# Kernel tuning notes

Measured on AMD Instinct MI355X. Metric: run time of the kernel, lower is better.

The kernel has to match this reference:

```python
import jax, jax.numpy as jnp
import numpy as np

GROUP_DIMS = (128, 64, 128, 64)  # per-group feature widths, sum = 384
ATTN_OUT = 64                    # per-group attention output width
B, W = 65536, 3                  # batch, words (4 groups * 3 words * 64 = 768 = linear_inner in-features)


def setup_inputs() -> dict:
    key = jax.random.key(0)
    keys = iter(jax.random.split(key, 64))
    s = 0.02
    inp = {"words": jax.random.normal(next(keys), (B, W, sum(GROUP_DIMS)), jnp.float32)}
    for g, d in enumerate(GROUP_DIMS):
        inp[f"wqkv{g}"] = jax.random.normal(next(keys), (d, 3 * d), jnp.float32) * s
        inp[f"bqkv{g}"] = jnp.zeros((3 * d,), jnp.float32)
        inp[f"wo{g}"] = jax.random.normal(next(keys), (d, ATTN_OUT), jnp.float32) * s
        inp[f"bo{g}"] = jnp.zeros((ATTN_OUT,), jnp.float32)
    inp["wi"] = jax.random.normal(next(keys), (ATTN_OUT * 12, 256), jnp.float32) * s
    inp["bi"] = jnp.zeros((256,), jnp.float32)
    inp["wout"] = jax.random.normal(next(keys), (256, 1), jnp.float32) * s
    inp["bout"] = jnp.zeros((1,), jnp.float32)
    return inp


def _group_attn(x, wqkv, bqkv, wo, bo, d):
    # x: [B, W, d] -> self-attention over W words within this feature group
    qkv = x @ wqkv + bqkv                      # [B, W, 3d]
    q, k, v = jnp.split(qkv, 3, axis=-1)       # each [B, W, d]
    scores = jnp.einsum('bqd,bkd->bqk', q, k) / jnp.sqrt(jnp.float32(d))
    attn = jax.nn.softmax(scores, axis=-1)     # [B, W, W]
    out = jnp.einsum('bqk,bkd->bqd', attn, v)  # [B, W, d]
    return out @ wo + bo                       # [B, W, ATTN_OUT]


def reference(words, wqkv0, bqkv0, wo0, bo0, wqkv1, bqkv1, wo1, bo1,
              wqkv2, bqkv2, wo2, bo2, wqkv3, bqkv3, wo3, bo3,
              wi, bi, wout, bout):
    gp = [(wqkv0, bqkv0, wo0, bo0), (wqkv1, bqkv1, wo1, bo1),
          (wqkv2, bqkv2, wo2, bo2), (wqkv3, bqkv3, wo3, bo3)]
    outs, start = [], 0
    for (wqkv, bqkv, wo, bo), d in zip(gp, GROUP_DIMS):
        outs.append(_group_attn(words[..., start:start + d], wqkv, bqkv, wo, bo, d))
        start += d
    cat = jnp.concatenate(outs, axis=-2)                 # [B, 12, 64]
    flat = jax.nn.relu(cat.reshape(cat.shape[0], -1))    # [B, 768]
    inner = jax.nn.relu(flat @ wi + bi)                  # [B, 256]
    return inner @ wout + bout                           # [B, 1]
```

## Files before the change

### kernel.cpp

```cpp
#include <hip/hip_runtime.h>

typedef _Float16 f16;
typedef _Float16 half8 __attribute__((ext_vector_type(8)));
typedef _Float16 half4 __attribute__((ext_vector_type(4)));
typedef __fp16 fp16x2 __attribute__((ext_vector_type(2)));
typedef float f32x4 __attribute__((ext_vector_type(4)));

#define BTOT 65536

static const size_t OFF_FLAT = 0;
static const size_t SZ_FLAT  = (size_t)BTOT * 768 * 2;
static const size_t OFF_WIT  = OFF_FLAT + SZ_FLAT;
static const size_t SZ_WIT   = (size_t)256 * 768 * 2;
static const size_t SZ_WT128 = (size_t)208 * 128 * 2;
static const size_t SZ_WT64  = (size_t)144 * 64 * 2;
static const size_t OFF_WT0  = OFF_WIT + SZ_WIT;
static const size_t OFF_WT1  = OFF_WT0 + SZ_WT128;
static const size_t OFF_WT2  = OFF_WT1 + SZ_WT64;
static const size_t OFF_WT3  = OFF_WT2 + SZ_WT128;
static const size_t OFF_CO   = OFF_WT3 + SZ_WT64;
static const size_t OFF_C    = OFF_CO + 256 * 4;

__device__ __forceinline__ half4 cvt4(float4 v) {
    fp16x2 lo = __builtin_amdgcn_cvt_pkrtz(v.x, v.y);
    fp16x2 hi = __builtin_amdgcn_cvt_pkrtz(v.z, v.w);
    half4 h;
    h[0] = (_Float16)lo[0]; h[1] = (_Float16)lo[1];
    h[2] = (_Float16)hi[0]; h[3] = (_Float16)hi[1];
    return h;
}

__device__ __forceinline__ void ldsbar() {
    asm volatile("s_waitcnt lgkmcnt(0)" ::: "memory");
    __builtin_amdgcn_s_barrier();
    __builtin_amdgcn_sched_barrier(0);
}

__global__ __launch_bounds__(256) void pk_fuse(
    const float* __restrict__ wq0, const float* __restrict__ bq0, const float* __restrict__ wo0, const float* __restrict__ bo0,
    const float* __restrict__ wq1, const float* __restrict__ bq1, const float* __restrict__ wo1, const float* __restrict__ bo1,
    const float* __restrict__ wq2, const float* __restrict__ bq2, const float* __restrict__ wo2, const float* __restrict__ bo2,
    const float* __restrict__ wq3, const float* __restrict__ bq3, const float* __restrict__ wo3, const float* __restrict__ bo3,
    f16* __restrict__ wT0, f16* __restrict__ wT1, f16* __restrict__ wT2, f16* __restrict__ wT3,
    float* __restrict__ coAll, float* __restrict__ cAll)
{
    const int g = blockIdx.y;
    const float* wqkv; const float* bqkv; const float* wo; const float* bo; f16* wT; int D;
    switch (g) {
        case 0:  wqkv = wq0; bqkv = bq0; wo = wo0; bo = bo0; wT = wT0; D = 128; break;
        case 1:  wqkv = wq1; bqkv = bq1; wo = wo1; bo = bo1; wT = wT1; D = 64;  break;
        case 2:  wqkv = wq2; bqkv = bq2; wo = wo2; bo = bo2; wT = wT2; D = 128; break;
        default: wqkv = wq3; bqkv = bq3; wo = wo3; bo = bo3; wT = wT3; D = 64;  break;
    }
    const int sh = (D == 128) ? 7 : 6;
    const int NT = (D + 81) / 16;
    const int NTD = (NT * 16) << sh;
    const int total = NTD + 65;
    const int o = blockIdx.x * 256 + threadIdx.x;
    if (o >= total) return;
    const int s3 = 3 * D;
    const float sc = rsqrtf((float)D);
    if (o < NTD) {
        const int n = o >> sh, k = o & (D - 1);
        float val = 0.f;
        if (n < D) {
            const float* a = wqkv + (size_t)k * s3;
            const float* b = wqkv + (size_t)n * s3 + D;
            float s = 0.f;
            for (int m = 0; m < D; ++m) s += a[m] * b[m];
            val = s * sc;
        } else if (n < D + 64) {
            const int j = n - D;
            const float* a = wqkv + (size_t)k * s3 + 2 * D;
            float s = 0.f;
            for (int m = 0; m < D; ++m) s += a[m] * wo[m * 64 + j];
            val = s;
        } else if (n == D + 64) {
            const float* a = wqkv + (size_t)k * s3;
            float s = 0.f;
            for (int m = 0; m < D; ++m) s += a[m] * bqkv[D + m];
            val = s * sc;
        } else if (n == D + 65) {
            const float* a = wqkv + (size_t)k * s3 + D;
            float s = 0.f;
            for (int m = 0; m < D; ++m) s += a[m] * bqkv[m];
            val = s * sc;
        }
        wT[o] = (f16)val;
    } else if (o < NTD + 64) {
        const int j = o - NTD;
        float s = 0.f;
        for (int m = 0; m < D; ++m) s += bqkv[2 * D + m] * wo[m * 64 + j];
        coAll[g * 64 + j] = s + bo[j];
    } else {
        float s = 0.f;
        for (int m = 0; m < D; ++m) s += bqkv[m] * bqkv[D + m];
        cAll[g] = s * sc;
    }
}

__global__ __launch_bounds__(256) void pk_wit(const float* __restrict__ wi, f16* __restrict__ wiT)
{
    int o = blockIdx.x * 256 + threadIdx.x;
    int n = o / 768, k = o - n * 768;
    wiT[o] = (f16)wi[k * 256 + n];
}

template<int D>
__device__ __forceinline__ void run_group(
    const float* __restrict__ words, const f16* __restrict__ wT,
    const float* __restrict__ coAll, const float* __restrict__ cAll, int gidx,
    f16* __restrict__ flat, int tile, int start, int gbase, int t, char* smem)
{
    constexpr int KST = D / 32;
    constexpr int NT  = (D + 81) / 16;
    constexpr int XP  = D + 8;
    constexpr int F4  = D / 4;
    constexpr int NLD = 48 * F4 / 256;

    f16 (*Xs)[XP]  = (f16(*)[XP])(smem);
    f16 (*Zs)[XP]  = (f16(*)[XP])(smem + (size_t)48 * XP * 2);
    f16 (*Zvo)[72] = (f16(*)[72])(smem + (size_t)96 * XP * 2);

    const int wc = t >> 6, lane = t & 63;
    const int lrow = lane & 15, lk = lane >> 4;
    const int r0 = t / F4, c4 = t - r0 * F4;
    const int b0 = tile * 16;

    const f16* wbase = wT + (size_t)lrow * D + lk * 8;

    {
        float4 v[NLD];
        #pragma unroll
        for (int i = 0; i < NLD; ++i) {
            int rr = r0 + i * (256 / F4);
            v[i] = *(const float4*)&words[(size_t)(b0 * 3 + rr) * 384 + start + c4 * 4];
        }
        #pragma unroll
        for (int i = 0; i < NLD; ++i) {
            int rr = r0 + i * (256 / F4);
            int prow = (rr % 3) * 16 + rr / 3;
            *(half4*)&Xs[prow][c4 * 4] = cvt4(v[i]);
        }
    }

    half8 bA[4], bB[4];
#define LOADB(BUF, KK)                                                          \
    { _Pragma("unroll")                                                         \
      for (int ci = 0; ci < 4; ++ci) {                                          \
          int ct = wc + ci * 4;                                                 \
          if (ct < NT) BUF[ci] = *(const half8*)&wbase[(size_t)ct * 16 * D + (KK) * 32]; \
      } }
    LOADB(bA, 0)

    ldsbar();

    {
        f32x4 acc[3][4];
        #pragma unroll
        for (int rt = 0; rt < 3; ++rt)
            #pragma unroll
            for (int ci = 0; ci < 4; ++ci) acc[rt][ci] = f32x4{0.f, 0.f, 0.f, 0.f};

#define MSTEP(BUF, KK)                                                          \
        { half8 a0 = *(const half8*)&Xs[ 0 + lrow][(KK) * 32 + lk * 8];         \
          half8 a1 = *(const half8*)&Xs[16 + lrow][(KK) * 32 + lk * 8];         \
          half8 a2 = *(const half8*)&Xs[32 + lrow][(KK) * 32 + lk * 8];         \
          _Pragma("unroll")                                                     \
          for (int ci = 0; ci < 4; ++ci) {                                      \
              int ct = wc + ci * 4;                                             \
              if (ct < NT) {                                                    \
                  acc[0][ci] = __builtin_amdgcn_mfma_f32_16x16x32_f16(a0, BUF[ci], acc[0][ci], 0, 0, 0); \
                  acc[1][ci] = __builtin_amdgcn_mfma_f32_16x16x32_f16(a1, BUF[ci], acc[1][ci], 0, 0, 0); \
                  acc[2][ci] = __builtin_amdgcn_mfma_f32_16x16x32_f16(a2, BUF[ci], acc[2][ci], 0, 0, 0); \
              } } }

        #pragma unroll
        for (int kp = 0; kp < KST / 2; ++kp) {
            LOADB(bB, 2 * kp + 1)
            MSTEP(bA, 2 * kp)
            if (2 * kp + 2 < KST) LOADB(bA, 2 * kp + 2)
            MSTEP(bB, 2 * kp + 1)
        }
#undef LOADB
#undef MSTEP

        #pragma unroll
        for (int ci = 0; ci < 4; ++ci) {
            int ct = wc + ci * 4;
            if (ct >= NT) continue;
            int n0 = ct * 16;
            if (n0 + 16 <= D) {
                #pragma unroll
                for (int rt = 0; rt < 3; ++rt)
                    #pragma unroll
                    for (int r = 0; r < 4; ++r)
                        Zs[rt * 16 + lk * 4 + r][n0 + lrow] = (f16)acc[rt][ci][r];
            } else if (n0 < D + 64) {
                #pragma unroll
                for (int rt = 0; rt < 3; ++rt)
                    #pragma unroll
                    for (int r = 0; r < 4; ++r)
                        Zvo[rt * 16 + lk * 4 + r][n0 - D + lrow] = (f16)acc[rt][ci][r];
            } else {
                if (lrow < 2) {
                    #pragma unroll
                    for (int rt = 0; rt < 3; ++rt)
                        #pragma unroll
                        for (int r = 0; r < 4; ++r)
                            ((float*)((char*)&Zs[rt * 16 + lk * 4 + r][D]))[lrow] = acc[rt][ci][r];
                }
            }
        }
    }
    ldsbar();

    if (wc < 3) {
        const float cval = cAll[gidx];
        f32x4 s0v = f32x4{0.f,0.f,0.f,0.f};
        f32x4 s1v = f32x4{0.f,0.f,0.f,0.f};
        f32x4 s2v = f32x4{0.f,0.f,0.f,0.f};
        #pragma unroll
        for (int kk = 0; kk < KST; ++kk) {
            half8 a  = *(const half8*)&Zs[wc * 16 + lrow][kk * 32 + lk * 8];
            half8 b0 = *(const half8*)&Xs[ 0 + lrow][kk * 32 + lk * 8];
            half8 b1 = *(const half8*)&Xs[16 + lrow][kk * 32 + lk * 8];
            half8 b2 = *(const half8*)&Xs[32 + lrow][kk * 32 + lk * 8];
            s0v = __builtin_amdgcn_mfma_f32_16x16x32_f16(a, b0, s0v, 0, 0, 0);
            s1v = __builtin_amdgcn_mfma_f32_16x16x32_f16(a, b1, s1v, 0, 0, 0);
            s2v = __builtin_amdgcn_mfma_f32_16x16x32_f16(a, b2, s2v, 0, 0, 0);
        }
        const int bb = lane & 15;
        const int rr3 = bb & 3;
#define EXT(q) ((rr3 & 2) ? ((rr3 & 1) ? q[3] : q[2]) : ((rr3 & 1) ? q[1] : q[0]))
        float xu = ((const float*)((const char*)&Zs[wc * 16 + bb][D]))[0];
        float sc0 = EXT(s0v) + xu + ((const float*)((const char*)&Zs[ 0 + bb][D]))[1] + cval;
        float sc1 = EXT(s1v) + xu + ((const float*)((const char*)&Zs[16 + bb][D]))[1] + cval;
        float sc2 = EXT(s2v) + xu + ((const float*)((const char*)&Zs[32 + bb][D]))[1] + cval;
#undef EXT
        float m = fmaxf(sc0, fmaxf(sc1, sc2));
        float e0 = __expf(sc0 - m), e1 = __expf(sc1 - m), e2 = __expf(sc2 - m);
        float inv = 1.0f / (e0 + e1 + e2);
        float p0 = e0 * inv, p1 = e1 * inv, p2 = e2 * inv;

        const int c8 = lane & 7;
        float cov[8];
        {
            float4 cA4 = *(const float4*)&coAll[gidx * 64 + c8 * 8];
            float4 cB4 = *(const float4*)&coAll[gidx * 64 + c8 * 8 + 4];
            cov[0]=cA4.x; cov[1]=cA4.y; cov[2]=cA4.z; cov[3]=cA4.w;
            cov[4]=cB4.x; cov[5]=cB4.y; cov[6]=cB4.z; cov[7]=cB4.w;
        }
        #pragma unroll
        for (int it = 0; it < 2; ++it) {
            int bb2 = (lane >> 3) + it * 8;
            int src = ((bb2 >> 2) << 4) | bb2;
            float q0 = __shfl(p0, src);
            float q1 = __shfl(p1, src);
            float q2 = __shfl(p2, src);
            half8 z0 = *(const half8*)&Zvo[ 0 + bb2][c8 * 8];
            half8 z1 = *(const half8*)&Zvo[16 + bb2][c8 * 8];
            half8 z2 = *(const half8*)&Zvo[32 + bb2][c8 * 8];
            half8 o;
            #pragma unroll
            for (int jj = 0; jj < 8; ++jj) {
                float v = q0 * (float)z0[jj] + q1 * (float)z1[jj] + q2 * (float)z2[jj]
                          + cov[jj];
                o[jj] = (f16)fmaxf(v, 0.f);
            }
            *(half8*)&flat[(size_t)(b0 + bb2) * 768 + gbase + wc * 64 + c8 * 8] = o;
        }
    }
}

__global__ __launch_bounds__(256) void k1(
    const float* __restrict__ words,
    const f16* __restrict__ wT0, const f16* __restrict__ wT1,
    const f16* __restrict__ wT2, const f16* __restrict__ wT3,
    const float* __restrict__ coAll, const float* __restrict__ cAll,
    f16* __restrict__ flat)
{
    extern __shared__ char smem[];
    const int t = threadIdx.x;
    const int tile = blockIdx.x;
    const int g = blockIdx.y;
    if (g == 0)
        run_group<128>(words, wT0, coAll, cAll, 0, flat, tile, 0,   0,   t, smem);
    else if (g == 1)
        run_group<64> (words, wT1, coAll, cAll, 1, flat, tile, 128, 192, t, smem);
    else if (g == 2)
        run_group<128>(words, wT2, coAll, cAll, 2, flat, tile, 192, 384, t, smem);
    else
        run_group<64> (words, wT3, coAll, cAll, 3, flat, tile, 320, 576, t, smem);
}

__global__ __launch_bounds__(512) void k2_mlp(
    const f16* __restrict__ flat, const f16* __restrict__ wiT,
    const float* __restrict__ bi, const float* __restrict__ wout, const float* __restrict__ bout,
    float* __restrict__ out)
{
    __shared__ f16 Wsh[256][72];
    __shared__ float part[128][2];
    __shared__ float bi_l[256], wo_l[256];

    const int t = threadIdx.x;
    const int b0 = blockIdx.x * 128;
    if (t < 256) { bi_l[t] = bi[t]; wo_l[t] = wout[t]; }

    const int wv = t >> 6, lane = t & 63;
    const int wr = wv >> 1, wc = wv & 1;
    const int lrow = lane & 15, lk = lane >> 4;

    const int pn = t >> 3, pc8 = t & 7;
    half8 wreg[4];
    #pragma unroll
    for (int j = 0; j < 4; ++j)
        wreg[j] = *(const half8*)&wiT[(size_t)(pn + j * 64) * 768 + pc8 * 8];

    const f16* arow0 = flat + (size_t)(b0 + wr * 32 + lrow) * 768;
    const f16* arow1 = flat + (size_t)(b0 + wr * 32 + 16 + lrow) * 768;

    f32x4 acc[2][8];
    #pragma unroll
    for (int i = 0; i < 2; ++i)
        #pragma unroll
        for (int j = 0; j < 8; ++j) acc[i][j] = f32x4{0.f, 0.f, 0.f, 0.f};

    for (int kc = 0; kc < 12; ++kc) {
        #pragma unroll
        for (int j = 0; j < 4; ++j)
            *(half8*)&Wsh[pn + j * 64][pc8 * 8] = wreg[j];
        ldsbar();
        if (kc + 1 < 12) {
            #pragma unroll
            for (int j = 0; j < 4; ++j)
                wreg[j] = *(const half8*)&wiT[(size_t)(pn + j * 64) * 768 + (kc + 1) * 64 + pc8 * 8];
        }
        #pragma unroll
        for (int ks = 0; ks < 2; ++ks) {
            half8 a0 = *(const half8*)&arow0[kc * 64 + ks * 32 + lk * 8];
            half8 a1 = *(const half8*)&arow1[kc * 64 + ks * 32 + lk * 8];
            #pragma unroll
            for (int ct = 0; ct < 8; ++ct) {
                half8 b = *(const half8*)&Wsh[wc * 128 + ct * 16 + lrow][ks * 32 + lk * 8];
                acc[0][ct] = __builtin_amdgcn_mfma_f32_16x16x32_f16(a0, b, acc[0][ct], 0, 0, 0);
                acc[1][ct] = __builtin_amdgcn_mfma_f32_16x16x32_f16(a1, b, acc[1][ct], 0, 0, 0);
            }
        }
        ldsbar();
    }

    float bo0 = bout[0];
    #pragma unroll
    for (int rt = 0; rt < 2; ++rt) {
        #pragma unroll
        for (int r = 0; r < 4; ++r) {
            float s = 0.f;
            #pragma unroll
            for (int ct = 0; ct < 8; ++ct) {
                int col = wc * 128 + ct * 16 + lrow;
                float v = acc[rt][ct][r] + bi_l[col];
                v = fmaxf(v, 0.f);
                s += v * wo_l[col];
            }
            s += __shfl_xor(s, 1, 64); s += __shfl_xor(s, 2, 64);
            s += __shfl_xor(s, 4, 64); s += __shfl_xor(s, 8, 64);
            if (lrow == 0) part[wr * 32 + rt * 16 + lk * 4 + r][wc] = s;
        }
    }
    ldsbar();
    if (t < 128) out[b0 + t] = part[t][0] + part[t][1] + bo0;
}

extern "C" void kernel_launch(void* const* d_in, const int* in_sizes, int n_in,
                              void* d_out, int out_size, void* d_ws, size_t ws_size,
                              hipStream_t stream)
{
    const float* words = (const float*)d_in[0];
    const float* wq[4] = {(const float*)d_in[1], (const float*)d_in[5], (const float*)d_in[9],  (const float*)d_in[13]};
    const float* bq[4] = {(const float*)d_in[2], (const float*)d_in[6], (const float*)d_in[10], (const float*)d_in[14]};
    const float* wo[4] = {(const float*)d_in[3], (const float*)d_in[7], (const float*)d_in[11], (const float*)d_in[15]};
    const float* bo[4] = {(const float*)d_in[4], (const float*)d_in[8], (const float*)d_in[12], (const float*)d_in[16]};
    const float* wi   = (const float*)d_in[17];
    const float* bi   = (const float*)d_in[18];
    const float* wout = (const float*)d_in[19];
    const float* bout = (const float*)d_in[20];

    char* ws = (char*)d_ws;
    f16*   flat = (f16*)(ws + OFF_FLAT);
    f16*   wiT  = (f16*)(ws + OFF_WIT);
    f16*   wT0  = (f16*)(ws + OFF_WT0);
    f16*   wT1  = (f16*)(ws + OFF_WT1);
    f16*   wT2  = (f16*)(ws + OFF_WT2);
    f16*   wT3  = (f16*)(ws + OFF_WT3);
    float* coA  = (float*)(ws + OFF_CO);
    float* cA   = (float*)(ws + OFF_C);

    pk_fuse<<<dim3(105, 4), 256, 0, stream>>>(
        wq[0], bq[0], wo[0], bo[0], wq[1], bq[1], wo[1], bo[1],
        wq[2], bq[2], wo[2], bo[2], wq[3], bq[3], wo[3], bo[3],
        wT0, wT1, wT2, wT3, coA, cA);
    pk_wit<<<768, 256, 0, stream>>>(wi, wiT);

    k1<<<dim3(4096, 4), 256, 33024, stream>>>(words, wT0, wT1, wT2, wT3, coA, cA, flat);

    k2_mlp<<<512, 512, 0, stream>>>(flat, wiT, bi, wout, bout, (float*)d_out);
}
```

Baseline: 206.2 us.

## Drop LDS staging in MLP kernel; load A and B fragments straight from global

The final MLP GEMM kernel no longer stages the inner weight matrix through shared memory with double-buffered register prefetch and per-chunk barriers. Each 256-thread block now handles 64 rows, and each wave reads its 64-column slice of the weights and the activation rows directly from global/L2 into MFMA fragments, computing a 4x4 tile of 16x16 outputs. This removes LDS traffic and barriers but relies on caches for weight reuse and issues more uncoalesced fragment loads. Partial dot products are reduced across four waves instead of two.

```diff
diff --git a/kernel.cpp b/kernel.cpp
--- a/kernel.cpp
+++ b/kernel.cpp
@@ -294,82 +294,72 @@
         run_group<64> (words, wT3, coAll, cAll, 3, flat, tile, 320, 576, t, smem);
 }
 
-__global__ __launch_bounds__(512) void k2_mlp(
+__global__ __launch_bounds__(256) void k2_mlp(
     const f16* __restrict__ flat, const f16* __restrict__ wiT,
     const float* __restrict__ bi, const float* __restrict__ wout, const float* __restrict__ bout,
     float* __restrict__ out)
 {
-    __shared__ f16 Wsh[256][72];
-    __shared__ float part[128][2];
+    __shared__ float part[64][4];
     __shared__ float bi_l[256], wo_l[256];
 
     const int t = threadIdx.x;
-    const int b0 = blockIdx.x * 128;
-    if (t < 256) { bi_l[t] = bi[t]; wo_l[t] = wout[t]; }
-
-    const int wv = t >> 6, lane = t & 63;
-    const int wr = wv >> 1, wc = wv & 1;
+    const int b0 = blockIdx.x * 64;
+    bi_l[t] = bi[t]; wo_l[t] = wout[t];
+
+    const int wc = t >> 6, lane = t & 63;
     const int lrow = lane & 15, lk = lane >> 4;
 
-    const int pn = t >> 3, pc8 = t & 7;
-    half8 wreg[4];
+    const f16* arow = flat + (size_t)(b0 + lrow) * 768 + lk * 8;
+    const f16* brow = wiT + (size_t)(wc * 64 + lrow) * 768 + lk * 8;
+
+    f32x4 acc[4][4];
     #pragma unroll
-    for (int j = 0; j < 4; ++j)
-        wreg[j] = *(const half8*)&wiT[(size_t)(pn + j * 64) * 768 + pc8 * 8];
-
-    const f16* arow0 = flat + (size_t)(b0 + wr * 32 + lrow) * 768;
-    const f16* arow1 = flat + (size_t)(b0 + wr * 32 + 16 + lrow) * 768;
-
-    f32x4 acc[2][8];
-    #pragma unroll
-    for (int i = 0; i < 2; ++i)
-        #pragma unroll
-        for (int j = 0; j < 8; ++j) acc[i][j] = f32x4{0.f, 0.f, 0.f, 0.f};
+    for (int i = 0; i < 4; ++i)
+        #pragma unroll
+        for (int j = 0; j < 4; ++j) acc[i][j] = f32x4{0.f, 0.f, 0.f, 0.f};
 
     for (int kc = 0; kc < 12; ++kc) {
         #pragma unroll
-        for (int j = 0; j < 4; ++j)
-            *(half8*)&Wsh[pn + j * 64][pc8 * 8] = wreg[j];
-        ldsbar();
-        if (kc + 1 < 12) {
-            #pragma unroll
-            for (int j = 0; j < 4; ++j)
-                wreg[j] = *(const half8*)&wiT[(size_t)(pn + j * 64) * 768 + (kc + 1) * 64 + pc8 * 8];
-        }
-        #pragma unroll
         for (int ks = 0; ks < 2; ++ks) {
-            half8 a0 = *(const half8*)&arow0[kc * 64 + ks * 32 + lk * 8];
-            half8 a1 = *(const half8*)&arow1[kc * 64 + ks * 32 + lk * 8];
-            #pragma unroll
-            for (int ct = 0; ct < 8; ++ct) {
-                half8 b = *(const half8*)&Wsh[wc * 128 + ct * 16 + lrow][ks * 32 + lk * 8];
-                acc[0][ct] = __builtin_amdgcn_mfma_f32_16x16x32_f16(a0, b, acc[0][ct], 0, 0, 0);
-                acc[1][ct] = __builtin_amdgcn_mfma_f32_16x16x32_f16(a1, b, acc[1][ct], 0, 0, 0);
-            }
-        }
-        ldsbar();
-    }
-
+            const int ko = kc * 64 + ks * 32;
+            half8 bf[4];
+            #pragma unroll
+            for (int ct = 0; ct < 4; ++ct)
+                bf[ct] = *(const half8*)&brow[(size_t)ct * 16 * 768 + ko];
+            half8 af[4];
+            #pragma unroll
+            for (int rt = 0; rt < 4; ++rt)
+                af[rt] = *(const half8*)&arow[(size_t)rt * 16 * 768 + ko];
+            #pragma unroll
+            for (int rt = 0; rt < 4; ++rt)
+                #pragma unroll
+                for (int ct = 0; ct < 4; ++ct)
+                    acc[rt][ct] = __builtin_amdgcn_mfma_f32_16x16x32_f16(af[rt], bf[ct], acc[rt][ct], 0, 0, 0);
+        }
+    }
+
+    ldsbar();
     float bo0 = bout[0];
     #pragma unroll
-    for (int rt = 0; rt < 2; ++rt) {
+    for (int rt = 0; rt < 4; ++rt) {
         #pragma unroll
         for (int r = 0; r < 4; ++r) {
             float s = 0.f;
             #pragma unroll
-            for (int ct = 0; ct < 8; ++ct) {
-                int col = wc * 128 + ct * 16 + lrow;
+            for (int ct = 0; ct < 4; ++ct) {
+                int col = wc * 64 + ct * 16 + lrow;
                 float v = acc[rt][ct][r] + bi_l[col];
                 v = fmaxf(v, 0.f);
                 s += v * wo_l[col];
             }
             s += __shfl_xor(s, 1, 64); s += __shfl_xor(s, 2, 64);
             s += __shfl_xor(s, 4, 64); s += __shfl_xor(s, 8, 64);
-            if (lrow == 0) part[wr * 32 + rt * 16 + lk * 4 + r][wc] = s;
+            if (lrow == 0) part[rt * 16 + lk * 4 + r][wc] = s;
         }
     }
     ldsbar();
-    if (t < 128) out[b0 + t] = part[t][0] + part[t][1] + bo0;
+    if (t < 64)
+        out[b0 + t] = part[t][0] + part[t][1] + part[t][2] + part[t][3] + bo0;
 }
 
 extern "C" void kernel_launch(void* const* d_in, const int* in_sizes, int n_in,
@@ -404,5 +394,5 @@
 
     k1<<<dim3(4096, 4), 256, 33024, stream>>>(words, wT0, wT1, wT2, wT3, coA, cA, flat);
 
-    k2_mlp<<<512, 512, 0, stream>>>(flat, wiT, bi, wout, bout, (float*)d_out);
-}
+    k2_mlp<<<1024, 256, 0, stream>>>(flat, wiT, bi, wout, bout, (float*)d_out);
+}
```

New measurement: 262.2 us. 1.27x slower.
